# Performance work log

Hardware: AMD Instinct MI355X
Metric: run time of the kernel (lower is better)

Reference implementation:

```python
import jax, jax.numpy as jnp
import numpy as np

EMBED_DIM = 1024
N_HEADS = 16
HEAD_DIM = EMBED_DIM // N_HEADS


def setup_inputs() -> dict:
    key = jax.random.key(0)
    ks = jax.random.split(key, 6)
    B, S, D = 4, 2048, EMBED_DIM
    s = 1.0 / np.sqrt(D)
    return {
        "x": jax.random.normal(ks[0], (B, S, D), dtype=jnp.float32),
        "Wq": jax.random.normal(ks[1], (D, D), dtype=jnp.float32) * s,
        "Wk": jax.random.normal(ks[2], (D, D), dtype=jnp.float32) * s,
        "Wv": jax.random.normal(ks[3], (D, D), dtype=jnp.float32) * s,
        "Wo": jax.random.normal(ks[4], (D, D), dtype=jnp.float32) * s,
        "bo": jax.random.normal(ks[5], (D,), dtype=jnp.float32) * 0.01,
    }


def reference(x, Wq, Wk, Wv, Wo, bo):
    B, S, D = x.shape
    H, Hd = N_HEADS, HEAD_DIM
    # q,k,v: [B,S,D] -> [B,H,S,Hd]
    def proj(W):
        return (x @ W.T).reshape(B, S, H, Hd).transpose(0, 2, 1, 3)
    q, k, v = proj(Wq), proj(Wk), proj(Wv)
    scores = jnp.einsum("bhqd,bhkd->bhqk", q, k) / jnp.sqrt(jnp.float32(Hd))
    attn = jax.nn.softmax(scores, axis=-1)  # dropout p=0.0 -> identity
    out = jnp.einsum("bhqk,bhkd->bhqd", attn, v)  # [B,H,S,Hd]
    out = out.transpose(0, 2, 1, 3).reshape(B, S, D)
    return out @ Wo.T + bo
```

## Files before the change

kernel.cpp:

```cpp
#include <hip/hip_runtime.h>


typedef unsigned short u16;
typedef unsigned int u32;
typedef float f32x4 __attribute__((ext_vector_type(4)));
typedef float f32x16 __attribute__((ext_vector_type(16)));
typedef short s16x8 __attribute__((ext_vector_type(8)));

#define DEVI __device__ __forceinline__

DEVI u16 f32_bf16(float f) {
  unsigned u = __float_as_uint(f);
  return (u16)((u + 0x7FFFu + ((u >> 16) & 1u)) >> 16);
}

DEVI u32 pack_pk(float a, float b) {
  u32 r;
  asm("v_cvt_pk_bf16_f32 %0, %1, %2" : "=v"(r) : "v"(a), "v"(b));
  return r;
}

DEVI void gload_lds16(const void* g, void* l) {
  __builtin_amdgcn_global_load_lds((const __attribute__((address_space(1))) void*)g,
                                   (__attribute__((address_space(3))) void*)l, 16, 0, 0);
}

#if __has_builtin(__builtin_amdgcn_permlane32_swap)
typedef int i32x2 __attribute__((ext_vector_type(2)));
DEVI void plswap(u32& a, u32& b, int hi) {
  i32x2 r = __builtin_amdgcn_permlane32_swap((int)a, (int)b, false, false);
  a = (u32)r[0];
  b = (u32)r[1];
}
DEVI float xhalf_add(float x) {
  i32x2 r = __builtin_amdgcn_permlane32_swap(__float_as_int(x), __float_as_int(x),
                                             false, false);
  return __int_as_float(r[0]) + __int_as_float(r[1]);
}
#else
DEVI void plswap(u32& a, u32& b, int hi) {
  u32 ta = (u32)__shfl_xor((int)a, 32);
  u32 tb = (u32)__shfl_xor((int)b, 32);
  u32 na = hi ? tb : a;
  u32 nb = hi ? b : ta;
  a = na;
  b = nb;
}
DEVI float xhalf_add(float x) { return x + __shfl_xor(x, 32); }
#endif

__global__ void cvt_all_kernel(const float* __restrict__ x, const float* __restrict__ wq,
                               const float* __restrict__ wk, const float* __restrict__ wv,
                               const float* __restrict__ wo, u16* __restrict__ x_bf,
                               u16* __restrict__ wcat, u16* __restrict__ wo_bf) {
  int bid = blockIdx.x;
  const float* src;
  u16* dst;
  int i;
  if (bid < 8192) {
    src = x; dst = x_bf; i = bid * 256 + threadIdx.x;
  } else {
    int m = (bid - 8192) >> 10;
    src = (m == 0) ? wq : (m == 1) ? wk : (m == 2) ? wv : wo;
    dst = (m < 3) ? (wcat + m * 1048576) : wo_bf;
    i = ((bid - 8192) & 1023) * 256 + threadIdx.x;
  }
  float4 v = ((const float4*)src)[i];
  ushort4 o;
  o.x = f32_bf16(v.x); o.y = f32_bf16(v.y);
  o.z = f32_bf16(v.z); o.w = f32_bf16(v.w);
  ((ushort4*)dst)[i] = o;
}

template <int MODE>
__global__ __launch_bounds__(256, 3) void gemm_bt(
    const u16* __restrict__ A, const u16* __restrict__ B, void* __restrict__ Cout,
    const float* __restrict__ bias, int M, int N, int K) {
  __shared__ u16 As[128 * 64];
  __shared__ u16 Bs[128 * 64];
  const int tid = threadIdx.x;
  const int lane = tid & 63;
  const int w = tid >> 6;
  const int wr = w >> 1, wc = w & 1;
  const int l15 = lane & 15, l4 = lane >> 4;
  const int swz = (l15 & 7) << 3;

  const int gx = gridDim.x;
  const int nwg = gx * gridDim.y;
  int ib = blockIdx.y * gx + blockIdx.x;
  int t = (ib & 7) * (nwg >> 3) + (ib >> 3);
  const int m0 = (t / gx) * 128, n0 = (t % gx) * 128;

  const int srow = w * 8 + (lane >> 3);
  const int scol = ((lane & 7) ^ (lane >> 3)) * 8;

  f32x4 acc[4][4] = {};

  for (int k0 = 0; k0 < K; k0 += 64) {
    __syncthreads();
#pragma unroll
    for (int i = 0; i < 4; ++i) {
      int cb = i * 256 + w * 64;
      int r = i * 32 + srow;
      gload_lds16(A + (size_t)(m0 + r) * K + k0 + scol, &As[cb * 8]);
      gload_lds16(B + (size_t)(n0 + r) * K + k0 + scol, &Bs[cb * 8]);
    }
    __syncthreads();

    s16x8 af[4][2], bf[4][2];
#pragma unroll
    for (int m = 0; m < 4; ++m)
#pragma unroll
      for (int ks = 0; ks < 2; ++ks)
        af[m][ks] = *(const s16x8*)&As[(wr * 64 + m * 16 + l15) * 64 +
                                       ((ks * 32 + l4 * 8) ^ swz)];
#pragma unroll
    for (int n = 0; n < 4; ++n)
#pragma unroll
      for (int ks = 0; ks < 2; ++ks)
        bf[n][ks] = *(const s16x8*)&Bs[(wc * 64 + n * 16 + l15) * 64 +
                                       ((ks * 32 + l4 * 8) ^ swz)];
    __builtin_amdgcn_s_setprio(1);
#pragma unroll
    for (int m = 0; m < 4; ++m)
#pragma unroll
      for (int n = 0; n < 4; ++n)
#pragma unroll
        for (int ks = 0; ks < 2; ++ks)
          acc[m][n] = __builtin_amdgcn_mfma_f32_16x16x32_bf16(af[m][ks], bf[n][ks],
                                                              acc[m][n], 0, 0, 0);
    __builtin_amdgcn_s_setprio(0);
  }

#pragma unroll
  for (int m = 0; m < 4; ++m) {
    int row = m0 + wr * 64 + m * 16 + l4 * 4;
#pragma unroll
    for (int n = 0; n < 4; ++n) {
      int col = n0 + wc * 64 + n * 16 + l15;
      if (MODE == 0) {
        u16* C = (u16*)Cout;
        float scale = (col < 1024) ? 0.18033688f : 1.0f;
#pragma unroll
        for (int j = 0; j < 4; ++j)
          C[(size_t)(row + j) * N + col] = f32_bf16(acc[m][n][j] * scale);
      } else {
        float* C = (float*)Cout;
        float bb = bias[col];
#pragma unroll
        for (int j = 0; j < 4; ++j)
          C[(size_t)(row + j) * N + col] = acc[m][n][j] + bb;
      }
    }
  }
}

__global__ __launch_bounds__(512, 4) void attn_kernel(const u16* __restrict__ QKV,
                                                      u16* __restrict__ AO) {
  __shared__ u16 Ks[2][128 * 64];
  __shared__ u16 Vt[2][64 * 128];
  const int tid = threadIdx.x;
  const int lane = tid & 63, w = tid >> 6;
  const int l31 = lane & 31, hi = lane >> 5;

  int ib = blockIdx.z * 128 + blockIdx.y * 8 + blockIdx.x;
  int tb = (ib & 7) * 64 + (ib >> 3);
  const int h = (tb >> 3) & 15, b = tb >> 7;
  const int rowbase = b * 2048;
  const int q0 = (tb & 7) * 256 + w * 32;

  s16x8 qa[4];
  {
    const u16* qp = QKV + (size_t)(rowbase + q0 + l31) * 3072 + h * 64 + hi * 8;
#pragma unroll
    for (int s = 0; s < 4; ++s) qa[s] = *(const s16x8*)(qp + s * 16);
  }

  const char* kbase = (const char*)(QKV + (size_t)rowbase * 3072 + 1024 + h * 64);
  const u16* vbase = QKV + (size_t)rowbase * 3072 + 2048 + h * 64;

  const int kgrow = lane >> 3;
  const int kgcol = ((lane & 7) * 16) ^ ((lane >> 3) << 4);
  const int kv = lane * 2;
  const int dv = w * 8;

  const int swzr = (l31 & 7) << 4;

  f32x16 o0 = {}, o1 = {};
  float ls0 = 0.f, ls1 = 0.f, ls2 = 0.f, ls3 = 0.f;

  {
#pragma unroll
    for (int c = 0; c < 2; ++c) {
      int chunk = w * 2 + c;
      gload_lds16(kbase + (chunk * 8 + kgrow) * 6144 + kgcol, &Ks[0][chunk * 512]);
    }
    const u16* vp = vbase + kv * 3072 + dv;
    s16x8 v0 = *(const s16x8*)vp, v1 = *(const s16x8*)(vp + 3072);
#pragma unroll
    for (int i = 0; i < 8; ++i) {
      int d = dv + i;
      *(u32*)((char*)&Vt[0][0] + d * 256 + ((kv * 2) ^ ((d & 7) << 4))) =
          (u32)(u16)v0[i] | ((u32)(u16)v1[i] << 16);
    }
  }
  __syncthreads();

  for (int kt = 0; kt < 16; ++kt) {
    const int cur = kt & 1;
    if (kt < 15) {
      const char* kb = kbase + (size_t)(kt + 1) * 128 * 6144;
#pragma unroll
      for (int c = 0; c < 2; ++c) {
        int chunk = w * 2 + c;
        gload_lds16(kb + (chunk * 8 + kgrow) * 6144 + kgcol, &Ks[cur ^ 1][chunk * 512]);
      }
    }

    const char* Kb = (const char*)&Ks[cur][0];
    const char* Vb = (const char*)&Vt[cur][0];
    s16x8 v0, v1;

#pragma unroll
    for (int sp = 0; sp < 2; ++sp) {
      f32x16 sa0 = {}, sa1 = {};
      __builtin_amdgcn_s_setprio(1);
#pragma unroll
      for (int s = 0; s < 4; ++s) {
        s16x8 kf = *(const s16x8*)(Kb + (sp * 64 + l31) * 128 + ((s * 32 + hi * 16) ^ swzr));
        sa0 = __builtin_amdgcn_mfma_f32_32x32x16_bf16(kf, qa[s], sa0, 0, 0, 0);
      }
#pragma unroll
      for (int s = 0; s < 4; ++s) {
        s16x8 kf = *(const s16x8*)(Kb + (sp * 64 + 32 + l31) * 128 + ((s * 32 + hi * 16) ^ swzr));
        sa1 = __builtin_amdgcn_mfma_f32_32x32x16_bf16(kf, qa[s], sa1, 0, 0, 0);
      }
      __builtin_amdgcn_s_setprio(0);

#pragma unroll
      for (int sub = 0; sub < 2; ++sub) {
        const int st = sp * 2 + sub;
        f32x16 s_acc = sub ? sa1 : sa0;

        u32 pk[8];
#pragma unroll
        for (int j = 0; j < 8; ++j) {
          float a = __builtin_amdgcn_exp2f(s_acc[2 * j]);
          float c = __builtin_amdgcn_exp2f(s_acc[2 * j + 1]);
          pk[j] = pack_pk(a, c);
          if ((j & 3) == 0) ls0 += a + c;
          else if ((j & 3) == 1) ls1 += a + c;
          else if ((j & 3) == 2) ls2 += a + c;
          else ls3 += a + c;
        }

        plswap(pk[0], pk[2], hi);
        plswap(pk[1], pk[3], hi);
        plswap(pk[4], pk[6], hi);
        plswap(pk[5], pk[7], hi);
        union { u32 u[4]; s16x8 v; } pb0, pb1;
        pb0.u[0] = pk[0]; pb0.u[1] = pk[1]; pb0.u[2] = pk[2]; pb0.u[3] = pk[3];
        pb1.u[0] = pk[4]; pb1.u[1] = pk[5]; pb1.u[2] = pk[6]; pb1.u[3] = pk[7];

        __builtin_amdgcn_s_setprio(1);
#pragma unroll
        for (int ks = 0; ks < 2; ++ks) {
          int cbyte = (st * 64 + ks * 32 + hi * 16) ^ swzr;
          s16x8 vf0 = *(const s16x8*)(Vb + l31 * 256 + cbyte);
          s16x8 vf1 = *(const s16x8*)(Vb + (32 + l31) * 256 + cbyte);
          s16x8 pf = ks ? pb1.v : pb0.v;
          o0 = __builtin_amdgcn_mfma_f32_32x32x16_bf16(vf0, pf, o0, 0, 0, 0);
          o1 = __builtin_amdgcn_mfma_f32_32x32x16_bf16(vf1, pf, o1, 0, 0, 0);
        }
        __builtin_amdgcn_s_setprio(0);
      }

      if (sp == 0 && kt < 15) {
        const u16* vp = vbase + ((kt + 1) * 128 + kv) * 3072 + dv;
        v0 = *(const s16x8*)vp;
        v1 = *(const s16x8*)(vp + 3072);
      }
    }

    if (kt < 15) {
#pragma unroll
      for (int i = 0; i < 8; ++i) {
        int d = dv + i;
        *(u32*)((char*)&Vt[cur ^ 1][0] + d * 256 + ((kv * 2) ^ ((d & 7) << 4))) =
            (u32)(u16)v0[i] | ((u32)(u16)v1[i] << 16);
      }
    }
    __syncthreads();
  }

  float lrow = xhalf_add((ls0 + ls1) + (ls2 + ls3));
  float inv = __builtin_amdgcn_rcpf(lrow);
  u16* op = AO + (size_t)(rowbase + q0 + l31) * 1024 + h * 64;
#pragma unroll
  for (int g = 0; g < 4; ++g) {
    ushort4 s0, s1;
    s0.x = f32_bf16(o0[g * 4 + 0] * inv);
    s0.y = f32_bf16(o0[g * 4 + 1] * inv);
    s0.z = f32_bf16(o0[g * 4 + 2] * inv);
    s0.w = f32_bf16(o0[g * 4 + 3] * inv);
    s1.x = f32_bf16(o1[g * 4 + 0] * inv);
    s1.y = f32_bf16(o1[g * 4 + 1] * inv);
    s1.z = f32_bf16(o1[g * 4 + 2] * inv);
    s1.w = f32_bf16(o1[g * 4 + 3] * inv);
    *(ushort4*)(op + g * 8 + 4 * hi) = s0;
    *(ushort4*)(op + 32 + g * 8 + 4 * hi) = s1;
  }
}

extern "C" void kernel_launch(void* const* d_in, const int* in_sizes, int n_in,
                              void* d_out, int out_size, void* d_ws, size_t ws_size,
                              hipStream_t stream) {
  const float* x = (const float*)d_in[0];
  const float* Wq = (const float*)d_in[1];
  const float* Wk = (const float*)d_in[2];
  const float* Wv = (const float*)d_in[3];
  const float* Wo = (const float*)d_in[4];
  const float* bo = (const float*)d_in[5];
  float* out = (float*)d_out;

  char* ws = (char*)d_ws;
  u16* x_bf = (u16*)ws;
  u16* Wcat = (u16*)(ws + 16777216);
  u16* Wo_bf = (u16*)(ws + 16777216 + 6291456);
  u16* QKV = (u16*)(ws + 16777216 + 6291456 + 2097152);
  u16* AO = (u16*)(ws + 16777216 + 6291456 + 2097152 + 50331648);

  cvt_all_kernel<<<12288, 256, 0, stream>>>(x, Wq, Wk, Wv, Wo, x_bf, Wcat, Wo_bf);

  gemm_bt<0><<<dim3(24, 64), 256, 0, stream>>>(x_bf, Wcat, QKV, nullptr, 8192, 3072, 1024);
  attn_kernel<<<dim3(8, 16, 4), 512, 0, stream>>>(QKV, AO);
  gemm_bt<1><<<dim3(8, 64), 256, 0, stream>>>(AO, Wo_bf, out, bo, 8192, 1024, 1024);
}
```

Baseline: 180.2 us.

## Use 256x256 eight-wave double-buffered GEMM for QKV projection

Replaces the 128x128 single-stage QKV projection GEMM with a new kernel using 256x256 output tiles, 8 waves per block, and double-buffered LDS. Global-to-LDS loads for the next K tiles are interleaved with the MFMA quarters. The larger tile raises arithmetic intensity and overlaps loads with compute. In exchange the grid shrinks to 384 blocks on 256 CUs, more LDS is used per block, and register pressure rises. The output-projection GEMM loses its template mode but otherwise keeps the same code.

```diff
diff --git a/kernel.cpp b/kernel.cpp
--- a/kernel.cpp
+++ b/kernel.cpp
@@ -72,9 +72,114 @@
   ((ushort4*)dst)[i] = o;
 }
 
-template <int MODE>
+__global__ __launch_bounds__(512, 2) void gemm8p(
+    const u16* __restrict__ A, const u16* __restrict__ B, u16* __restrict__ Cout,
+    int M, int N, int K) {
+  __shared__ u16 SA[2][2][128 * 64];
+  __shared__ u16 SB[2][2][128 * 64];
+  const int tid = threadIdx.x;
+  const int lane = tid & 63, w = tid >> 6;
+  const int wm = w >> 2, wn = w & 3;
+  const int l15 = lane & 15, l4 = lane >> 4;
+  const int swz = (l15 & 7) << 3;
+
+  const int gx = gridDim.x;
+  const int nwg = gx * gridDim.y;
+  int ib = blockIdx.y * gx + blockIdx.x;
+  int t = (ib & 7) * (nwg >> 3) + (ib >> 3);
+  const int m0 = (t / gx) * 256, n0 = (t % gx) * 256;
+
+  const int sr8 = lane >> 3;
+  const int scol = ((lane & 7) ^ sr8) * 8;
+
+  f32x4 acc[8][4] = {};
+  const int NT = K >> 6;
+
+  auto STG = [&](const u16* G, int grow0, u16* ldsbase, int kk) {
+#pragma unroll
+    for (int L = 0; L < 2; ++L) {
+      int rl = L * 64 + w * 8;
+      gload_lds16(G + (size_t)(grow0 + rl + sr8) * K + kk + scol, ldsbase + rl * 64);
+    }
+  };
+
+  STG(B, n0, &SB[0][0][0], 0);
+  STG(B, n0 + 128, &SB[0][1][0], 0);
+  STG(A, m0, &SA[0][0][0], 0);
+  STG(A, m0 + 128, &SA[0][1][0], 0);
+  STG(B, n0, &SB[1][0][0], 64);
+  STG(B, n0 + 128, &SB[1][1][0], 64);
+  asm volatile("s_waitcnt vmcnt(4)" ::: "memory");
+  asm volatile("s_barrier" ::: "memory");
+
+  for (int kt = 0; kt < NT; ++kt) {
+    const int p = kt & 1;
+    const u16* sa = &SA[p][wm][0];
+    const u16* sb = &SB[p][wn >> 1][(wn & 1) * 4096];
+    const int kk1 = (kt + 1) << 6, kk2 = (kt + 2) << 6;
+    const bool st1 = (kt + 1) < NT, st2 = (kt + 2) < NT;
+
+    s16x8 bf[4][2];
+#pragma unroll
+    for (int q = 0; q < 4; ++q) {
+      if (q == 0) {
+#pragma unroll
+        for (int nf = 0; nf < 4; ++nf)
+#pragma unroll
+          for (int ks = 0; ks < 2; ++ks)
+            bf[nf][ks] = *(const s16x8*)&sb[(nf * 16 + l15) * 64 +
+                                            ((ks * 32 + l4 * 8) ^ swz)];
+      }
+      s16x8 af[2][2];
+#pragma unroll
+      for (int m2 = 0; m2 < 2; ++m2)
+#pragma unroll
+        for (int ks = 0; ks < 2; ++ks)
+          af[m2][ks] = *(const s16x8*)&sa[((q * 2 + m2) * 16 + l15) * 64 +
+                                          ((ks * 32 + l4 * 8) ^ swz)];
+      if (q == 0) { if (st1) STG(A, m0, &SA[p ^ 1][0][0], kk1); }
+      else if (q == 1) { if (st1) STG(A, m0 + 128, &SA[p ^ 1][1][0], kk1); }
+      else if (q == 2) { if (st2) STG(B, n0, &SB[p][0][0], kk2); }
+      else { if (st2) STG(B, n0 + 128, &SB[p][1][0], kk2); }
+
+      asm volatile("s_barrier" ::: "memory");
+      __builtin_amdgcn_s_setprio(1);
+#pragma unroll
+      for (int m2 = 0; m2 < 2; ++m2)
+#pragma unroll
+        for (int nf = 0; nf < 4; ++nf)
+#pragma unroll
+          for (int ks = 0; ks < 2; ++ks)
+            acc[q * 2 + m2][nf] = __builtin_amdgcn_mfma_f32_16x16x32_bf16(
+                af[m2][ks], bf[nf][ks], acc[q * 2 + m2][nf], 0, 0, 0);
+      __builtin_amdgcn_s_setprio(0);
+      if (q == 3) {
+        if (kt == NT - 2) {
+          asm volatile("s_waitcnt vmcnt(0)" ::: "memory");
+        } else if (kt < NT - 2) {
+          asm volatile("s_waitcnt vmcnt(4)" ::: "memory");
+        }
+      }
+      asm volatile("s_barrier" ::: "memory");
+    }
+  }
+
+#pragma unroll
+  for (int mf = 0; mf < 8; ++mf) {
+    int row = m0 + wm * 128 + mf * 16 + l4 * 4;
+#pragma unroll
+    for (int nf = 0; nf < 4; ++nf) {
+      int col = n0 + wn * 64 + nf * 16 + l15;
+      float scale = (col < 1024) ? 0.18033688f : 1.0f;
+#pragma unroll
+      for (int j = 0; j < 4; ++j)
+        Cout[(size_t)(row + j) * N + col] = f32_bf16(acc[mf][nf][j] * scale);
+    }
+  }
+}
+
 __global__ __launch_bounds__(256, 3) void gemm_bt(
-    const u16* __restrict__ A, const u16* __restrict__ B, void* __restrict__ Cout,
+    const u16* __restrict__ A, const u16* __restrict__ B, float* __restrict__ Cout,
     const float* __restrict__ bias, int M, int N, int K) {
   __shared__ u16 As[128 * 64];
   __shared__ u16 Bs[128 * 64];
@@ -138,19 +243,10 @@
 #pragma unroll
     for (int n = 0; n < 4; ++n) {
       int col = n0 + wc * 64 + n * 16 + l15;
-      if (MODE == 0) {
-        u16* C = (u16*)Cout;
-        float scale = (col < 1024) ? 0.18033688f : 1.0f;
-#pragma unroll
-        for (int j = 0; j < 4; ++j)
-          C[(size_t)(row + j) * N + col] = f32_bf16(acc[m][n][j] * scale);
-      } else {
-        float* C = (float*)Cout;
-        float bb = bias[col];
-#pragma unroll
-        for (int j = 0; j < 4; ++j)
-          C[(size_t)(row + j) * N + col] = acc[m][n][j] + bb;
-      }
+      float bb = bias[col];
+#pragma unroll
+      for (int j = 0; j < 4; ++j)
+        Cout[(size_t)(row + j) * N + col] = acc[m][n][j] + bb;
     }
   }
 }
@@ -332,7 +428,7 @@
 
   cvt_all_kernel<<<12288, 256, 0, stream>>>(x, Wq, Wk, Wv, Wo, x_bf, Wcat, Wo_bf);
 
-  gemm_bt<0><<<dim3(24, 64), 256, 0, stream>>>(x_bf, Wcat, QKV, nullptr, 8192, 3072, 1024);
+  gemm8p<<<dim3(12, 32), 512, 0, stream>>>(x_bf, Wcat, QKV, 8192, 3072, 1024);
   attn_kernel<<<dim3(8, 16, 4), 512, 0, stream>>>(QKV, AO);
-  gemm_bt<1><<<dim3(8, 64), 256, 0, stream>>>(AO, Wo_bf, out, bo, 8192, 1024, 1024);
-}
+  gemm_bt<<<dim3(8, 64), 256, 0, stream>>>(AO, Wo_bf, out, bo, 8192, 1024, 1024);
+}
```

New measurement: 193.8 us. 1.08x slower.
